# Kernel optimization log

Measured on AMD Instinct MI355X. Metric: run time of the kernel, lower is better.

## Reference

```python
import jax, jax.numpy as jnp
import numpy as np

IN_FEATURES = 4096
OUT_FEATURES = 4096
BLOCK_SIZE = 64
LOWRANK_DIM = 64
BATCH = 4096  # flat batch of tokens


def _butterfly_forward_indices(out_features, in_features, block_size):
    """Replicates lean_transformer.get_butterfly_indices forward_indices for the
    square case where butterfly_size == num_blocks (here 4096/64 = 64).
    Block (p, q) is active iff p ^ q has popcount <= 1 (identity + all log2(n) butterfly factors).
    """
    nob = out_features // block_size  # num output blocks
    nib = in_features // block_size   # num input blocks
    p = np.arange(nob)[:, None]
    q = np.arange(nib)[None, :]
    x = p ^ q
    layout = (x & (x - 1)) == 0  # True when x == 0 or x is a power of two
    a_out = int(layout.sum(1)[0])  # active input blocks per output block
    a_in = int(layout.sum(0)[0])   # active output blocks per input block
    input_block_index = np.nonzero(layout)[1].reshape(nob, a_out)
    output_block_index = np.nonzero(layout.T)[1].reshape(nib, a_in)
    # for output block p and its s-th active input block j, find which of j's
    # active output slots points back to p
    gathered = output_block_index[input_block_index]  # [nob, a_out, a_in]
    active = np.argmax(gathered == np.arange(nob)[:, None, None], axis=-1)
    return (input_block_index * a_in + active).astype(np.int32)


def setup_inputs() -> dict:
    key = jax.random.key(0)
    k1, k2, k3, k4 = jax.random.split(key, 4)
    std = float(np.sqrt(2.0 / (5 * min(OUT_FEATURES, IN_FEATURES))))
    fwd_idx = _butterfly_forward_indices(OUT_FEATURES, IN_FEATURES, BLOCK_SIZE)
    a_in = fwd_idx.size // (IN_FEATURES // BLOCK_SIZE)  # active blocks per input
    return {
        "input": jax.random.normal(k1, (BATCH, IN_FEATURES), jnp.float32),
        "weight": jax.random.normal(k2, (IN_FEATURES, a_in, BLOCK_SIZE), jnp.float32) * std,
        "lowrank_first": jax.random.normal(k3, (LOWRANK_DIM, IN_FEATURES), jnp.float32) * std,
        "lowrank_second": jax.random.normal(k4, (OUT_FEATURES, LOWRANK_DIM), jnp.float32) * std,
        "forward_indices": jnp.asarray(fwd_idx),  # [num_output_blocks, a_out] int32
    }


def _butterfly_matmul(x, weight, forward_indices):
    # x: [B, in_features]; weight: [in_features, a_in, block_size]
    batch = x.shape[0]
    in_f, a_in, bs = weight.shape
    nib = in_f // bs
    xb = x.reshape(batch, nib, bs)                     # [B, nib, bs]
    w = weight.reshape(nib, bs, a_in, bs)              # [nib, bs, a_in, bs]
    # per-input-block contributions to each of its a_in candidate output blocks
    contrib = jnp.einsum("bjk,jkac->bjac", xb, w)      # [B, nib, a_in, bs]
    contrib = contrib.reshape(batch, nib * a_in, bs)
    # gather the contributions feeding each output block and accumulate
    out = contrib[:, forward_indices, :].sum(axis=2)   # [B, nob, bs]
    return out.reshape(batch, -1)                      # [B, out_features]


def reference(input, weight, lowrank_first, lowrank_second, forward_indices):
    out = _butterfly_matmul(input, weight, forward_indices)
    # low-rank correction: F.linear(F.linear(x, W1), W2, out)
    out = out + (input @ lowrank_first.T) @ lowrank_second.T
    return out
```

## Files before the change

kernel.cpp:

```cpp
#include <hip/hip_runtime.h>
#include <hip/hip_bf16.h>


#define DEVINL __device__ __forceinline__

typedef __attribute__((ext_vector_type(8))) short bfx8;
typedef __attribute__((ext_vector_type(4))) float fx4;

DEVINL short f2bf(float f) {
  unsigned u = __builtin_bit_cast(unsigned, f);
  unsigned r = 0x7FFFu + ((u >> 16) & 1u);
  return (short)((u + r) >> 16);
}

DEVINL int swzb(int row, int kbyte) { return (row << 7) + (kbyte ^ ((row & 7) << 4)); }

DEVINL void gload16(const void* g, void* l) {
  __builtin_amdgcn_global_load_lds(
      (const __attribute__((address_space(1))) unsigned int*)g,
      (__attribute__((address_space(3))) unsigned int*)l, 16, 0, 0);
}

__global__ __launch_bounds__(256) void prep_all_kern(
    const float* __restrict__ weight, const float* __restrict__ w1,
    const float* __restrict__ w2, const int* __restrict__ fwd,
    const float* __restrict__ x, unsigned short* __restrict__ bmat,
    unsigned short* __restrict__ w1b, unsigned short* __restrict__ xb) {
  int cid = blockIdx.x, tid = threadIdx.x;
  if (cid >= 576) {
    int gid = (cid - 576) * 256 + tid;
    int b = gid >> 9, c8 = gid & 511;
    int j = c8 >> 3, c0 = (c8 & 7) << 3;
    const float* src = x + (size_t)b * 4096 + j * 64 + c0;
    fx4 v0 = *(const fx4*)src;
    fx4 v1 = *(const fx4*)(src + 4);
    bfx8 o;
    o[0] = f2bf(v0[0]); o[1] = f2bf(v0[1]); o[2] = f2bf(v0[2]); o[3] = f2bf(v0[3]);
    o[4] = f2bf(v1[0]); o[5] = f2bf(v1[1]); o[6] = f2bf(v1[2]); o[7] = f2bf(v1[3]);
    size_t off = (size_t)j * 262144 + (size_t)b * 64 + ((((c0 << 1) ^ ((b & 7) << 4))) >> 1);
    *(bfx8*)(xb + off) = o;
    return;
  }
  if (cid < 512) {
    int p = cid >> 3, t = cid & 7;
    unsigned short* dst = bmat + (size_t)cid * 4096;
    if (t < 7) {
      int idx = fwd[p * 7 + t];
      int j = idx / 7, a = idx - j * 7;
      int k = tid >> 2, n0 = (tid & 3) << 4;
      const float* src = weight + ((size_t)(j * 64 + k) * 7 + a) * 64 + n0;
#pragma unroll
      for (int e = 0; e < 16; ++e) {
        int n = n0 + e;
        dst[(n << 6) + ((((k << 1) ^ ((n & 7) << 4))) >> 1)] = f2bf(src[e]);
      }
    } else {
      int n = tid >> 2, r0 = (tid & 3) << 4;
      const float* src = w2 + ((size_t)(p * 64 + n)) * 64 + r0;
#pragma unroll
      for (int e = 0; e < 16; ++e) {
        int k = r0 + e;
        dst[(n << 6) + ((((k << 1) ^ ((n & 7) << 4))) >> 1)] = f2bf(src[e]);
      }
    }
  } else {
    int jc = cid - 512;
    unsigned short* dst = w1b + (size_t)jc * 4096;
    int r = tid >> 2, k0 = (tid & 3) << 4;
    const float* src = w1 + (size_t)r * 4096 + jc * 64 + k0;
#pragma unroll
    for (int e = 0; e < 16; ++e) {
      int k = k0 + e;
      dst[(r << 6) + ((((k << 1) ^ ((r & 7) << 4))) >> 1)] = f2bf(src[e]);
    }
  }
}

__global__ __launch_bounds__(256) void compute_t_split(const unsigned short* __restrict__ xb,
                                                       const unsigned short* __restrict__ w1b,
                                                       float* __restrict__ part) {
  __shared__ char smem[32768];
  int rt = blockIdx.x >> 3, kc = blockIdx.x & 7;
  int tid = threadIdx.x, lane = tid & 63, w = tid >> 6;
  int lr = lane & 15, lkb = (lane >> 4) << 4;

  auto stage = [&](int jc, int buf) {
    const unsigned short* sa = xb + (size_t)(kc * 8 + jc) * 262144 + (size_t)rt * 4096;
    const unsigned short* sb = w1b + (size_t)(kc * 8 + jc) * 4096;
    char* da = smem + buf * 8192;
    char* db = smem + 16384 + buf * 8192;
#pragma unroll
    for (int i = 0; i < 2; ++i) {
      gload16(sa + tid * 8 + i * 2048, da + tid * 16 + i * 4096);
      gload16(sb + tid * 8 + i * 2048, db + tid * 16 + i * 4096);
    }
  };

  fx4 acc[4] = {};
  stage(0, 0);
#pragma unroll 1
  for (int jc = 0; jc < 8; ++jc) {
    __syncthreads();
    int cur = jc & 1;
    if (jc < 7) stage(jc + 1, cur ^ 1);
    const char* ab = smem + cur * 8192;
    const char* bb = smem + 16384 + cur * 8192;
#pragma unroll
    for (int kk = 0; kk < 2; ++kk) {
      bfx8 af = *(const bfx8*)(ab + swzb(w * 16 + lr, kk * 64 + lkb));
#pragma unroll
      for (int ni = 0; ni < 4; ++ni) {
        bfx8 bf = *(const bfx8*)(bb + swzb(ni * 16 + lr, kk * 64 + lkb));
        acc[ni] = __builtin_amdgcn_mfma_f32_16x16x32_bf16(af, bf, acc[ni], 0, 0, 0);
      }
    }
  }
  float* pb = part + (size_t)kc * 262144 + (size_t)rt * 4096;
#pragma unroll
  for (int ni = 0; ni < 4; ++ni)
#pragma unroll
    for (int r = 0; r < 4; ++r) {
      int row = w * 16 + (lane >> 4) * 4 + r;
      pb[(size_t)row * 64 + ni * 16 + lr] = acc[ni][r];
    }
}

__global__ __launch_bounds__(256) void reduce_t_kern(const float* __restrict__ part,
                                                     unsigned short* __restrict__ tb) {
  int gid = blockIdx.x * 256 + threadIdx.x;
  int b = gid >> 3, c0 = (gid & 7) << 3;
  const float* pp = part + (size_t)b * 64 + c0;
  fx4 s0 = {0.f, 0.f, 0.f, 0.f}, s1 = {0.f, 0.f, 0.f, 0.f};
#pragma unroll
  for (int kc = 0; kc < 8; ++kc) {
    s0 += *(const fx4*)(pp + (size_t)kc * 262144);
    s1 += *(const fx4*)(pp + (size_t)kc * 262144 + 4);
  }
  bfx8 o;
#pragma unroll
  for (int e = 0; e < 4; ++e) { o[e] = f2bf(s0[e]); o[e + 4] = f2bf(s1[e]); }
  *(bfx8*)(tb + (size_t)b * 64 + ((((c0 << 1) ^ ((b & 7) << 4))) >> 1)) = o;
}

__global__ __launch_bounds__(256, 4) void butterfly_mp(
    const unsigned short* __restrict__ xb, const unsigned short* __restrict__ tb,
    const unsigned short* __restrict__ bmat, const int* __restrict__ fwd,
    float* __restrict__ out) {
  __shared__ char smem[32768];
  int bid = blockIdx.x;
  int wid = (bid & 7) * 128 + (bid >> 3);
  int mt = wid >> 4, pg = wid & 15;
  int tid = threadIdx.x, lane = tid & 63, w = tid >> 6;
  int lr = lane & 15, lkb = (lane >> 4) << 4;

  auto stage = [&](int s, int buf) {
    int qq = s >> 3, tt = s & 7;
    int ps = pg * 4 + qq;
    const unsigned short* srcA;
    if (tt < 7) {
      int j = fwd[ps * 7 + tt] / 7;
      srcA = xb + ((size_t)j * 4096 + mt * 64) * 64;
    } else {
      srcA = tb + (size_t)(mt * 64) * 64;
    }
    char* da = smem + buf * 8192;
    gload16(srcA + tid * 8, da + tid * 16);
    gload16(srcA + tid * 8 + 2048, da + tid * 16 + 4096);
    const unsigned short* srcB = bmat + ((size_t)(ps * 8 + tt)) * 4096;
    char* db = smem + 16384 + buf * 8192;
    gload16(srcB + tid * 8, db + tid * 16);
    gload16(srcB + tid * 8 + 2048, db + tid * 16 + 4096);
  };

  fx4 acc[4][4] = {};
  stage(0, 0);
#pragma unroll
  for (int q = 0; q < 4; ++q) {
#pragma unroll 1
    for (int t = 0; t < 8; ++t) {
      int s = q * 8 + t;
      __syncthreads();
      if (s < 31) stage(s + 1, (s + 1) & 1);
      const char* ab = smem + (s & 1) * 8192;
      const char* bb = smem + 16384 + (s & 1) * 8192;
#pragma unroll
      for (int kk = 0; kk < 2; ++kk) {
        bfx8 af = *(const bfx8*)(ab + swzb(w * 16 + lr, kk * 64 + lkb));
#pragma unroll
        for (int ni = 0; ni < 4; ++ni) {
          bfx8 bf = *(const bfx8*)(bb + swzb(ni * 16 + lr, kk * 64 + lkb));
          acc[q][ni] = __builtin_amdgcn_mfma_f32_16x16x32_bf16(af, bf, acc[q][ni], 0, 0, 0);
        }
      }
    }
  }

  size_t rbase = (size_t)(mt * 64 + w * 16) * 4096 + pg * 256;
#pragma unroll
  for (int q = 0; q < 4; ++q)
#pragma unroll
    for (int ni = 0; ni < 4; ++ni)
#pragma unroll
      for (int r = 0; r < 4; ++r)
        out[rbase + (size_t)((lane >> 4) * 4 + r) * 4096 + q * 64 + ni * 16 + lr] =
            acc[q][ni][r];
}

__global__ void naive_t_kern(const float* __restrict__ x, const float* __restrict__ w1,
                             float* __restrict__ t) {
  int gid = blockIdx.x * 256 + threadIdx.x;
  int b = gid >> 6, r = gid & 63;
  const float* xr = x + (size_t)b * 4096;
  const float* wr = w1 + (size_t)r * 4096;
  float s = 0.f;
  for (int k = 0; k < 4096; ++k) s += xr[k] * wr[k];
  t[gid] = s;
}

__global__ void naive_out_kern(const float* __restrict__ x, const float* __restrict__ weight,
                               const float* __restrict__ w2, const int* __restrict__ fwd,
                               const float* __restrict__ t, float* __restrict__ out) {
  size_t gid = (size_t)blockIdx.x * 256 + threadIdx.x;
  int b = (int)(gid >> 12), o = (int)(gid & 4095);
  int p = o >> 6, n = o & 63;
  float s = 0.f;
  for (int si = 0; si < 7; ++si) {
    int idx = fwd[p * 7 + si], j = idx / 7, a = idx - j * 7;
    const float* xr = x + (size_t)b * 4096 + j * 64;
    for (int k = 0; k < 64; ++k)
      s += xr[k] * weight[((size_t)(j * 64 + k) * 7 + a) * 64 + n];
  }
  const float* tr = t + (size_t)b * 64;
  const float* w2r = w2 + (size_t)o * 64;
  for (int r = 0; r < 64; ++r) s += tr[r] * w2r[r];
  out[gid] = s;
}

extern "C" void kernel_launch(void* const* d_in, const int* in_sizes, int n_in,
                              void* d_out, int out_size, void* d_ws, size_t ws_size,
                              hipStream_t stream) {
  const float* x = (const float*)d_in[0];
  const float* weight = (const float*)d_in[1];
  const float* w1 = (const float*)d_in[2];
  const float* w2 = (const float*)d_in[3];
  const int* fwd = (const int*)d_in[4];
  float* out = (float*)d_out;

  const size_t XB_E = 16777216;
  const size_t TB_E = 262144;
  const size_t BM_E = 2097152;
  const size_t W1_E = 262144;
  const size_t BASE_B = (XB_E + TB_E + BM_E + W1_E) * 2;

  if (ws_size >= BASE_B) {
    unsigned short* xb = (unsigned short*)d_ws;
    unsigned short* tb = xb + XB_E;
    unsigned short* bmat = tb + TB_E;
    unsigned short* w1b = bmat + BM_E;
    float* part = out;
    prep_all_kern<<<8768, 256, 0, stream>>>(weight, w1, w2, fwd, x, bmat, w1b, xb);
    compute_t_split<<<512, 256, 0, stream>>>(xb, w1b, part);
    reduce_t_kern<<<128, 256, 0, stream>>>(part, tb);
    butterfly_mp<<<1024, 256, 0, stream>>>(xb, tb, bmat, fwd, out);
  } else {
    float* t = (float*)d_ws;
    naive_t_kern<<<1024, 256, 0, stream>>>(x, w1, t);
    naive_out_kern<<<65536, 256, 0, stream>>>(x, weight, w2, fwd, t, out);
  }
}
```

Measured before the change: 68.67 us.

## Triple-buffer A tiles with deeper prefetch and explicit vmcnt waits in butterfly GEMM

Splits the tile staging into separate A and B loads, giving the A (activation) tiles a three-slot ring buffer that is prefetched two steps ahead while B stays double-buffered. The plain __syncthreads is replaced by raw s_barrier plus explicit s_waitcnt vmcnt counts, so only the loads needed for the current step must land before compute. The goal is to hide global-to-LDS latency better. The cost is 8 KB more LDS per block, which could limit occupancy, and hand-tuned wait counts that must match the issue order exactly.

```diff
diff --git a/kernel.cpp b/kernel.cpp
--- a/kernel.cpp
+++ b/kernel.cpp
@@ -142,18 +142,18 @@
   *(bfx8*)(tb + (size_t)b * 64 + ((((c0 << 1) ^ ((b & 7) << 4))) >> 1)) = o;
 }
 
-__global__ __launch_bounds__(256, 4) void butterfly_mp(
+__global__ __launch_bounds__(256, 4) void butterfly_mp3(
     const unsigned short* __restrict__ xb, const unsigned short* __restrict__ tb,
     const unsigned short* __restrict__ bmat, const int* __restrict__ fwd,
     float* __restrict__ out) {
-  __shared__ char smem[32768];
+  __shared__ char smem[40960];
   int bid = blockIdx.x;
   int wid = (bid & 7) * 128 + (bid >> 3);
   int mt = wid >> 4, pg = wid & 15;
   int tid = threadIdx.x, lane = tid & 63, w = tid >> 6;
   int lr = lane & 15, lkb = (lane >> 4) << 4;
 
-  auto stage = [&](int s, int buf) {
+  auto stageA = [&](int s, int slot) {
     int qq = s >> 3, tt = s & 7;
     int ps = pg * 4 + qq;
     const unsigned short* srcA;
@@ -163,26 +163,43 @@
     } else {
       srcA = tb + (size_t)(mt * 64) * 64;
     }
-    char* da = smem + buf * 8192;
+    char* da = smem + slot * 8192;
     gload16(srcA + tid * 8, da + tid * 16);
     gload16(srcA + tid * 8 + 2048, da + tid * 16 + 4096);
+  };
+  auto stageB = [&](int s, int slot) {
+    int qq = s >> 3, tt = s & 7;
+    int ps = pg * 4 + qq;
     const unsigned short* srcB = bmat + ((size_t)(ps * 8 + tt)) * 4096;
-    char* db = smem + 16384 + buf * 8192;
+    char* db = smem + 24576 + slot * 8192;
     gload16(srcB + tid * 8, db + tid * 16);
     gload16(srcB + tid * 8 + 2048, db + tid * 16 + 4096);
   };
 
   fx4 acc[4][4] = {};
-  stage(0, 0);
+  stageA(0, 0);
+  stageB(0, 0);
+  stageA(1, 1);
+
+  int ca = 0;
 #pragma unroll
   for (int q = 0; q < 4; ++q) {
 #pragma unroll 1
     for (int t = 0; t < 8; ++t) {
       int s = q * 8 + t;
-      __syncthreads();
-      if (s < 31) stage(s + 1, (s + 1) & 1);
-      const char* ab = smem + (s & 1) * 8192;
-      const char* bb = smem + 16384 + (s & 1) * 8192;
+      __builtin_amdgcn_s_barrier();
+      __builtin_amdgcn_sched_barrier(0);
+      if (s < 31) stageB(s + 1, (s + 1) & 1);
+      if (s < 30) stageA(s + 2, ca >= 1 ? ca - 1 : ca + 2);
+      if (s < 30)       asm volatile("s_waitcnt vmcnt(6)" ::: "memory");
+      else if (s == 30) asm volatile("s_waitcnt vmcnt(4)" ::: "memory");
+      else              asm volatile("s_waitcnt vmcnt(0)" ::: "memory");
+      __builtin_amdgcn_sched_barrier(0);
+      __builtin_amdgcn_s_barrier();
+      __builtin_amdgcn_sched_barrier(0);
+
+      const char* ab = smem + ca * 8192;
+      const char* bb = smem + 24576 + (s & 1) * 8192;
 #pragma unroll
       for (int kk = 0; kk < 2; ++kk) {
         bfx8 af = *(const bfx8*)(ab + swzb(w * 16 + lr, kk * 64 + lkb));
@@ -192,6 +209,7 @@
           acc[q][ni] = __builtin_amdgcn_mfma_f32_16x16x32_bf16(af, bf, acc[q][ni], 0, 0, 0);
         }
       }
+      ca = (ca >= 2) ? 0 : ca + 1;
     }
   }
 
@@ -261,7 +279,7 @@
     prep_all_kern<<<8768, 256, 0, stream>>>(weight, w1, w2, fwd, x, bmat, w1b, xb);
     compute_t_split<<<512, 256, 0, stream>>>(xb, w1b, part);
     reduce_t_kern<<<128, 256, 0, stream>>>(part, tb);
-    butterfly_mp<<<1024, 256, 0, stream>>>(xb, tb, bmat, fwd, out);
+    butterfly_mp3<<<1024, 256, 0, stream>>>(xb, tb, bmat, fwd, out);
   } else {
     float* t = (float*)d_ws;
     naive_t_kern<<<1024, 256, 0, stream>>>(x, w1, t);
```

Result: slower. 71.49 us (+4.1%).

## Keep B-matrix for one output block resident in LDS across eight M tiles

Applied to the files above, without the earlier changes.

The butterfly kernel changes from tiling over four output blocks per workgroup to one output block per workgroup. All eight B tiles for that block stay resident in LDS (64KB) while the kernel streams eight 64-row M tiles of A through a double buffer. This cuts repeated B loads and halves the grid to 512 workgroups. In exchange it uses 80KB of LDS, lowers occupancy to 2 blocks per CU, and narrows the output tile.

```diff
diff --git a/kernel.cpp b/kernel.cpp
--- a/kernel.cpp
+++ b/kernel.cpp
@@ -142,68 +142,68 @@
   *(bfx8*)(tb + (size_t)b * 64 + ((((c0 << 1) ^ ((b & 7) << 4))) >> 1)) = o;
 }
 
-__global__ __launch_bounds__(256, 4) void butterfly_mp(
+__global__ __launch_bounds__(256, 2) void butterfly_br(
     const unsigned short* __restrict__ xb, const unsigned short* __restrict__ tb,
     const unsigned short* __restrict__ bmat, const int* __restrict__ fwd,
     float* __restrict__ out) {
-  __shared__ char smem[32768];
+  __shared__ char smem[81920];
   int bid = blockIdx.x;
-  int wid = (bid & 7) * 128 + (bid >> 3);
-  int mt = wid >> 4, pg = wid & 15;
+  int xcd = bid & 7, local = bid >> 3;
+  int p = xcd * 8 + (local & 7);
+  int mtg = local >> 3;
   int tid = threadIdx.x, lane = tid & 63, w = tid >> 6;
   int lr = lane & 15, lkb = (lane >> 4) << 4;
 
-  auto stage = [&](int s, int buf) {
-    int qq = s >> 3, tt = s & 7;
-    int ps = pg * 4 + qq;
+  auto stageA = [&](int s, int buf) {
+    int mi = s >> 3, tt = s & 7;
     const unsigned short* srcA;
     if (tt < 7) {
-      int j = fwd[ps * 7 + tt] / 7;
-      srcA = xb + ((size_t)j * 4096 + mt * 64) * 64;
+      int j = fwd[p * 7 + tt] / 7;
+      srcA = xb + ((size_t)j * 4096 + (mtg * 8 + mi) * 64) * 64;
     } else {
-      srcA = tb + (size_t)(mt * 64) * 64;
-    }
-    char* da = smem + buf * 8192;
+      srcA = tb + (size_t)((mtg * 8 + mi) * 64) * 64;
+    }
+    char* da = smem + 65536 + buf * 8192;
     gload16(srcA + tid * 8, da + tid * 16);
     gload16(srcA + tid * 8 + 2048, da + tid * 16 + 4096);
-    const unsigned short* srcB = bmat + ((size_t)(ps * 8 + tt)) * 4096;
-    char* db = smem + 16384 + buf * 8192;
+  };
+
+#pragma unroll
+  for (int t = 0; t < 8; ++t) {
+    const unsigned short* srcB = bmat + ((size_t)(p * 8 + t)) * 4096;
+    char* db = smem + t * 8192;
     gload16(srcB + tid * 8, db + tid * 16);
     gload16(srcB + tid * 8 + 2048, db + tid * 16 + 4096);
-  };
-
-  fx4 acc[4][4] = {};
-  stage(0, 0);
-#pragma unroll
-  for (int q = 0; q < 4; ++q) {
+  }
+  stageA(0, 0);
+
+#pragma unroll 1
+  for (int mi = 0; mi < 8; ++mi) {
+    fx4 acc[4] = {};
 #pragma unroll 1
     for (int t = 0; t < 8; ++t) {
-      int s = q * 8 + t;
+      int s = mi * 8 + t;
       __syncthreads();
-      if (s < 31) stage(s + 1, (s + 1) & 1);
-      const char* ab = smem + (s & 1) * 8192;
-      const char* bb = smem + 16384 + (s & 1) * 8192;
+      if (s < 63) stageA(s + 1, (s + 1) & 1);
+      const char* ab = smem + 65536 + (s & 1) * 8192;
+      const char* bb = smem + t * 8192;
 #pragma unroll
       for (int kk = 0; kk < 2; ++kk) {
         bfx8 af = *(const bfx8*)(ab + swzb(w * 16 + lr, kk * 64 + lkb));
 #pragma unroll
         for (int ni = 0; ni < 4; ++ni) {
           bfx8 bf = *(const bfx8*)(bb + swzb(ni * 16 + lr, kk * 64 + lkb));
-          acc[q][ni] = __builtin_amdgcn_mfma_f32_16x16x32_bf16(af, bf, acc[q][ni], 0, 0, 0);
+          acc[ni] = __builtin_amdgcn_mfma_f32_16x16x32_bf16(af, bf, acc[ni], 0, 0, 0);
         }
       }
     }
-  }
-
-  size_t rbase = (size_t)(mt * 64 + w * 16) * 4096 + pg * 256;
-#pragma unroll
-  for (int q = 0; q < 4; ++q)
+    size_t rbase = (size_t)((mtg * 8 + mi) * 64 + w * 16) * 4096 + p * 64;
 #pragma unroll
     for (int ni = 0; ni < 4; ++ni)
 #pragma unroll
       for (int r = 0; r < 4; ++r)
-        out[rbase + (size_t)((lane >> 4) * 4 + r) * 4096 + q * 64 + ni * 16 + lr] =
-            acc[q][ni][r];
+        out[rbase + (size_t)((lane >> 4) * 4 + r) * 4096 + ni * 16 + lr] = acc[ni][r];
+  }
 }
 
 __global__ void naive_t_kern(const float* __restrict__ x, const float* __restrict__ w1,
@@ -261,7 +261,7 @@
     prep_all_kern<<<8768, 256, 0, stream>>>(weight, w1, w2, fwd, x, bmat, w1b, xb);
     compute_t_split<<<512, 256, 0, stream>>>(xb, w1b, part);
     reduce_t_kern<<<128, 256, 0, stream>>>(part, tb);
-    butterfly_mp<<<1024, 256, 0, stream>>>(xb, tb, bmat, fwd, out);
+    butterfly_br<<<512, 256, 0, stream>>>(xb, tb, bmat, fwd, out);
   } else {
     float* t = (float*)d_ws;
     naive_t_kern<<<1024, 256, 0, stream>>>(x, w1, t);
```

Measured after the change: 73.64 us. +7.2%, slower.
